# Kernel optimization log

Hardware: AMD Instinct MI355X
Metric: run time of the kernel (lower is better)

The kernel has to match this reference:

```python
import jax, jax.numpy as jnp
import numpy as np

M, K, N = 1024, 8192, 8192
PACK = 16  # 16 two-bit codes per int32 word


def _pack_ternary(codes):
    # codes: (N, K) int32 with values in {0,1,3} -> (N, K//16) int32
    c = codes.reshape(N, K // PACK, PACK).astype(jnp.uint32)
    shifts = (jnp.arange(PACK, dtype=jnp.uint32) * 2)
    packed = jnp.sum(c << shifts, axis=-1, dtype=jnp.uint32)
    return jax.lax.bitcast_convert_type(packed, jnp.int32)


def setup_inputs() -> dict:
    key = jax.random.key(0)
    kx, kw, kb = jax.random.split(key, 3)
    x = jax.random.normal(kx, (M, K), dtype=jnp.float16)
    # ternary codes drawn from {0,1,3} (code 2 is unused by the format)
    vals = jnp.array([0, 1, 3], dtype=jnp.int32)
    codes = vals[jax.random.randint(kw, (N, K), 0, 3)]
    packed_w = _pack_ternary(codes)
    bias = jax.random.normal(kb, (N,), dtype=jnp.float16)
    return {"x": x, "packed_w": packed_w, "bias": bias}


def _unpack(packed_w):
    # (N, K//16) int32 -> (N, K) fp16 weights with values in {0,1,3}
    shifts = jnp.arange(PACK, dtype=jnp.int32) * 2
    w = (packed_w[:, :, None] >> shifts) & 3  # mask keeps low 2 bits even with arithmetic shift
    return w.reshape(packed_w.shape[0], -1).astype(jnp.float16)


def reference(x, packed_w, bias):
    w = _unpack(packed_w)  # (N, K)
    # Y = X W^T + b, fp32 accumulation as in the CUDA/Triton GEMM, fp16 output
    y = jnp.einsum('mk,nk->mn', x, w, preferred_element_type=jnp.float32)
    y = y.astype(jnp.float16) + bias
    return y
```

## Files before the change

### kernel.cpp

```cpp
#include <hip/hip_runtime.h>
#include <hip/hip_fp16.h>
#include <stdint.h>

#define M_DIM 1024
#define N_DIM 8192
#define K_DIM 8192
#define KP    (K_DIM / 16)

#define BM 128
#define BN 128
#define BK 64
#define NTHREADS 256
#define B_STRIDE 144

#define MT_STRIDE 2097152
#define KT_STRIDE 16384

typedef _Float16 half8   __attribute__((ext_vector_type(8)));
typedef __fp16   fp16x2  __attribute__((ext_vector_type(2)));
typedef float    f32x4   __attribute__((ext_vector_type(4)));
typedef float    f32x16  __attribute__((ext_vector_type(16)));

__device__ __forceinline__ uint32_t cvt2(float a, float b) {
  fp16x2 p = __builtin_amdgcn_cvt_pkrtz(a, b);
  return __builtin_bit_cast(uint32_t, p);
}

__device__ __forceinline__ half8 dec_frag(uint32_t word, uint32_t sh) {
  const uint32_t T = 0x42063C00u;
  uint32_t h  = (word >> sh) & 0xFFFFu;
  uint32_t W  = (h & 0x3333u) | ((h << 14) & 0x33330000u);
  uint32_t c0 = __builtin_amdgcn_perm(0u, W, 0x04040200u);
  uint32_t c1 = __builtin_amdgcn_perm(0u, W, 0x04040301u);
  uint32_t s0 = (c0 * 0x1001u) & 0x03030303u;
  uint32_t s1 = (c1 * 0x1001u) & 0x03030303u;
  uint32_t P0 = __builtin_amdgcn_perm(0u, T, s0);
  uint32_t P1 = __builtin_amdgcn_perm(0u, T, s1);
  uint4 v;
  v.x = __builtin_amdgcn_perm(P0, 0u, 0x05000400u);
  v.y = __builtin_amdgcn_perm(P0, 0u, 0x07000600u);
  v.z = __builtin_amdgcn_perm(P1, 0u, 0x05000400u);
  v.w = __builtin_amdgcn_perm(P1, 0u, 0x07000600u);
  return __builtin_bit_cast(half8, v);
}

__global__ __launch_bounds__(256)
void cvt_x_t(const float* __restrict__ x, char* __restrict__ xhT) {
  __shared__ __align__(16) char st[16384];
  const int b  = blockIdx.x;
  const int mt = b >> 7, kt = b & 127;
  const int t  = threadIdx.x;
#pragma unroll
  for (int p = 0; p < 8; ++p) {
    int f   = t + 256 * p;
    int R   = f >> 4;
    int cc4 = f & 15;
    float4 v = *(const float4*)(x + (size_t)(mt * 128 + R) * K_DIM + kt * 64 + cc4 * 4);
    uint32_t w0 = cvt2(v.x, v.y), w1 = cvt2(v.z, v.w);
    int c8 = cc4 >> 1, hh = cc4 & 1;
    int i32 = R >> 5, r = R & 31, ks = c8 >> 1, q = c8 & 1;
    *(uint2*)(st + i32 * 4096 + ks * 1024 + q * 512 + r * 16 + hh * 8) = make_uint2(w0, w1);
  }
  __syncthreads();
  char* outb = xhT + (size_t)mt * MT_STRIDE + (size_t)kt * KT_STRIDE;
#pragma unroll
  for (int e = 0; e < 4; ++e) {
    int d = (e * 256 + t) * 16;
    *(uint4*)(outb + d) = *(const uint4*)(st + d);
  }
}

__global__ __launch_bounds__(NTHREADS, 2)
void ternary_gemm_dc(const char* __restrict__ xhT,
                     const int*  __restrict__ pw,
                     const float* __restrict__ bias,
                     float*       __restrict__ out) {
  __shared__ __align__(16) char stg[2 * 2048];

  const int tid  = threadIdx.x;
  const int lane = tid & 63;
  const int w    = tid >> 6;
  const int wm   = w >> 1, wn = w & 1;
  const int bid  = blockIdx.x;
  const int mt   = bid & 7;
  const int bm   = mt * BM;
  const int bn   = (bid >> 3) * BN;

  const char* pA[2];
#pragma unroll
  for (int i = 0; i < 2; ++i)
    pA[i] = xhT + (size_t)mt * MT_STRIDE + (wm * 2 + i) * 4096 + lane * 16;

  const int rT = tid >> 1, hT = tid & 1;
  const int2* gB = (const int2*)pw + (size_t)(bn + rT) * (KP / 2) + hT;
  const int stOff = rT * 16 + hT * 8;

  int rowOff[2];
#pragma unroll
  for (int j = 0; j < 2; ++j)
    rowOff[j] = (wn * 64 + j * 32 + (lane & 31)) * 16;
  const uint32_t sh = (lane >> 5) * 16;

  f32x16 acc[2][2];
#pragma unroll
  for (int i = 0; i < 2; ++i)
#pragma unroll
    for (int j = 0; j < 2; ++j) acc[i][j] = (f32x16)(0.f);

  const int NT = K_DIM / BK;

  *(int2*)(stg + stOff) = gB[0];
  half8 aA[2][4], aB[2][4];
#pragma unroll
  for (int i = 0; i < 2; ++i)
#pragma unroll
    for (int ks = 0; ks < 4; ++ks)
      aA[i][ks] = *(const half8*)(pA[i] + ks * 1024);
#pragma unroll
  for (int i = 0; i < 2; ++i) pA[i] += KT_STRIDE;
  int2 wcur = gB[2];
  __syncthreads();

  auto step = [&](half8 (&aC)[2][4], half8 (&aN)[2][4], int cur, int kt) {
#pragma unroll
    for (int i = 0; i < 2; ++i)
#pragma unroll
      for (int ks = 0; ks < 4; ++ks)
        aN[i][ks] = *(const half8*)(pA[i] + ks * 1024);
    if (kt < NT - 2) {
#pragma unroll
      for (int i = 0; i < 2; ++i) pA[i] += KT_STRIDE;
    }
    int kn2 = (kt + 2 < NT) ? (kt + 2) : (NT - 1);
    int2 wnxt = gB[kn2 * 2];

    uint32_t wr0[4], wr1[4];
    *(uint4*)wr0 = *(const uint4*)(stg + cur * 2048 + rowOff[0]);
    *(uint4*)wr1 = *(const uint4*)(stg + cur * 2048 + rowOff[1]);
    *(int2*)(stg + (cur ^ 1) * 2048 + stOff) = wcur;

#pragma unroll
    for (int ks = 0; ks < 4; ++ks) {
      half8 bf0 = dec_frag(wr0[ks], sh);
      half8 bf1 = dec_frag(wr1[ks], sh);
      acc[0][0] = __builtin_amdgcn_mfma_f32_32x32x16_f16(aC[0][ks], bf0, acc[0][0], 0, 0, 0);
      acc[0][1] = __builtin_amdgcn_mfma_f32_32x32x16_f16(aC[0][ks], bf1, acc[0][1], 0, 0, 0);
      acc[1][0] = __builtin_amdgcn_mfma_f32_32x32x16_f16(aC[1][ks], bf0, acc[1][0], 0, 0, 0);
      acc[1][1] = __builtin_amdgcn_mfma_f32_32x32x16_f16(aC[1][ks], bf1, acc[1][1], 0, 0, 0);
    }

    __syncthreads();
    wcur = wnxt;
  };

  for (int kt = 0; kt < NT; kt += 2) {
    step(aA, aB, 0, kt);
    step(aB, aA, 1, kt + 1);
  }

#pragma unroll
  for (int j = 0; j < 2; ++j) {
    int n = bn + wn * 64 + j * 32 + (lane & 31);
    __half hb = __float2half_rn(bias[n]);
#pragma unroll
    for (int i = 0; i < 2; ++i) {
      int mbase = bm + wm * 64 + i * 32 + 4 * (lane >> 5);
#pragma unroll
      for (int reg = 0; reg < 16; ++reg) {
        int m = mbase + (reg & 3) + 8 * (reg >> 2);
        __half hy = __float2half_rn(acc[i][j][reg]);
        out[(size_t)m * N_DIM + n] = __half2float(__hadd(hy, hb));
      }
    }
  }
}

__device__ __forceinline__ uint32_t unpack_pair16(uint32_t u, int p) {
  uint32_t c0 = (u >> (4 * p)) & 3u;
  uint32_t c1 = (u >> (4 * p + 2)) & 3u;
  uint32_t lo = (c0 & 1u) * 0x3C00u + (c0 >> 1) * 0x0600u;
  uint32_t hi = (c1 & 1u) * 0x3C00u + (c1 >> 1) * 0x0600u;
  return lo | (hi << 16);
}

__global__ __launch_bounds__(NTHREADS, 2)
void ternary_gemm(const float* __restrict__ x,
                  const int*   __restrict__ pw,
                  const float* __restrict__ bias,
                  float*       __restrict__ out) {
  __shared__ __align__(16) char AsB[128 * B_STRIDE];
  __shared__ __align__(16) char BsB[128 * B_STRIDE];

  const int tid  = threadIdx.x;
  const int lane = tid & 63;
  const int w    = tid >> 6;
  const int wm   = w >> 1, wn = w & 1;
  const int bid  = blockIdx.x;
  const int bm   = (bid & 7) * 128;
  const int bn   = (bid >> 3) * 128;

  const int rT = tid >> 1, hT = tid & 1;
  const float* gA = x + (size_t)(bm + rT) * K_DIM + hT * 32;
  char* const  lA = AsB + rT * B_STRIDE + hT * 64;
  const int2* gB = (const int2*)pw + (size_t)(bn + rT) * (KP / 2) + hT;
  char* dBp[4];
#pragma unroll
  for (int h = 0; h < 4; ++h)
    dBp[h] = BsB + rT * B_STRIDE + (hT * 4 + h) * 16;

  int offA[4][2], offB[4][2];
#pragma unroll
  for (int i = 0; i < 4; ++i)
#pragma unroll
    for (int ks = 0; ks < 2; ++ks) {
      int c = ks * 4 + (lane >> 4);
      offA[i][ks] = (wm * 64 + i * 16 + (lane & 15)) * B_STRIDE + c * 16;
      offB[i][ks] = (wn * 64 + i * 16 + (lane & 15)) * B_STRIDE + c * 16;
    }

  f32x4 acc[4][4];
#pragma unroll
  for (int i = 0; i < 4; ++i)
#pragma unroll
    for (int j = 0; j < 4; ++j)
      acc[i][j] = (f32x4){0.f, 0.f, 0.f, 0.f};

  const int NT = K_DIM / BK;
  for (int kt = 0; kt < NT; ++kt) {
    __syncthreads();
    int2 wcur = gB[kt * 2];
    float4 av[8];
#pragma unroll
    for (int v = 0; v < 8; ++v) av[v] = *(const float4*)(gA + kt * BK + v * 4);
    uint32_t d0[8], d1[8];
#pragma unroll
    for (int p = 0; p < 8; ++p) d0[p] = unpack_pair16((uint32_t)wcur.x, p);
#pragma unroll
    for (int p = 0; p < 8; ++p) d1[p] = unpack_pair16((uint32_t)wcur.y, p);
    *(uint4*)dBp[0] = make_uint4(d0[0], d0[1], d0[2], d0[3]);
    *(uint4*)dBp[1] = make_uint4(d0[4], d0[5], d0[6], d0[7]);
    *(uint4*)dBp[2] = make_uint4(d1[0], d1[1], d1[2], d1[3]);
    *(uint4*)dBp[3] = make_uint4(d1[4], d1[5], d1[6], d1[7]);
#pragma unroll
    for (int v = 0; v < 4; ++v) {
      uint4 aw;
      aw.x = cvt2(av[2 * v].x, av[2 * v].y);
      aw.y = cvt2(av[2 * v].z, av[2 * v].w);
      aw.z = cvt2(av[2 * v + 1].x, av[2 * v + 1].y);
      aw.w = cvt2(av[2 * v + 1].z, av[2 * v + 1].w);
      *(uint4*)(lA + v * 16) = aw;
    }
    __syncthreads();
#pragma unroll
    for (int ks = 0; ks < 2; ++ks) {
      half8 af[4], bf[4];
#pragma unroll
      for (int i = 0; i < 4; ++i) af[i] = *(const half8*)(AsB + offA[i][ks]);
#pragma unroll
      for (int j = 0; j < 4; ++j) bf[j] = *(const half8*)(BsB + offB[j][ks]);
#pragma unroll
      for (int i = 0; i < 4; ++i)
#pragma unroll
        for (int j = 0; j < 4; ++j)
          acc[i][j] = __builtin_amdgcn_mfma_f32_16x16x32_f16(af[i], bf[j], acc[i][j], 0, 0, 0);
    }
  }
#pragma unroll
  for (int j = 0; j < 4; ++j) {
    int n = bn + wn * 64 + j * 16 + (lane & 15);
    __half hb = __float2half_rn(bias[n]);
#pragma unroll
    for (int i = 0; i < 4; ++i) {
      int m0 = bm + wm * 64 + i * 16 + (lane >> 4) * 4;
#pragma unroll
      for (int r = 0; r < 4; ++r) {
        __half hy = __float2half_rn(acc[i][j][r]);
        out[(size_t)(m0 + r) * N_DIM + n] = __half2float(__hadd(hy, hb));
      }
    }
  }
}

extern "C" void kernel_launch(void* const* d_in, const int* in_sizes, int n_in,
                              void* d_out, int out_size, void* d_ws, size_t ws_size,
                              hipStream_t stream) {
  (void)in_sizes; (void)n_in; (void)out_size;
  const float* x    = (const float*)d_in[0];
  const int*   pwp  = (const int*)d_in[1];
  const float* bias = (const float*)d_in[2];
  float*       outp = (float*)d_out;

  const size_t need = (size_t)M_DIM * K_DIM * 2;
  if (ws_size >= need) {
    char* xhT = (char*)d_ws;
    cvt_x_t<<<8 * 128, 256, 0, stream>>>(x, xhT);
    dim3 grid((M_DIM / BM) * (N_DIM / BN));
    ternary_gemm_dc<<<grid, NTHREADS, 0, stream>>>(xhT, pwp, bias, outp);
  } else {
    dim3 grid((M_DIM / 128) * (N_DIM / 128));
    ternary_gemm<<<grid, NTHREADS, 0, stream>>>(x, pwp, bias, outp);
  }
}
```

Before: 237.0 us.

## Add weight repack pass and LDS-free single-wave 64x64 tile GEMM kernel

Adds a repack kernel that rearranges the packed ternary weights into a per-32-row-tile, per-k-step layout in workspace, so each lane can load its fragment directly. A new single-wavefront GEMM kernel with 64x64 tiles then streams both operands straight from global memory into registers with double buffering, removing shared memory staging and barriers. This adds an extra repack pass and workspace, and gives up the inter-wave data reuse of the 128x128 tile, so global and L2 traffic per output grows. The new path runs only when the workspace is large enough.

Measured after the change: 263.9 us. 1.11x slower.

```diff
diff --git a/kernel.cpp b/kernel.cpp
--- a/kernel.cpp
+++ b/kernel.cpp
@@ -7,14 +7,12 @@
 #define K_DIM 8192
 #define KP    (K_DIM / 16)
 
-#define BM 128
-#define BN 128
 #define BK 64
-#define NTHREADS 256
 #define B_STRIDE 144
 
 #define MT_STRIDE 2097152
 #define KT_STRIDE 16384
+#define BW_OFF    ((size_t)16 * 1024 * 1024)
 
 typedef _Float16 half8   __attribute__((ext_vector_type(8)));
 typedef __fp16   fp16x2  __attribute__((ext_vector_type(2)));
@@ -26,9 +24,8 @@
   return __builtin_bit_cast(uint32_t, p);
 }
 
-__device__ __forceinline__ half8 dec_frag(uint32_t word, uint32_t sh) {
+__device__ __forceinline__ half8 dec_h(uint32_t h) {
   const uint32_t T = 0x42063C00u;
-  uint32_t h  = (word >> sh) & 0xFFFFu;
   uint32_t W  = (h & 0x3333u) | ((h << 14) & 0x33330000u);
   uint32_t c0 = __builtin_amdgcn_perm(0u, W, 0x04040200u);
   uint32_t c1 = __builtin_amdgcn_perm(0u, W, 0x04040301u);
@@ -70,7 +67,124 @@
   }
 }
 
-__global__ __launch_bounds__(NTHREADS, 2)
+__global__ __launch_bounds__(256)
+void repack_w(const int* __restrict__ pw, char* __restrict__ bws) {
+  const int nt  = blockIdx.x & 255;
+  const int ktg = blockIdx.x >> 8;
+  const int r   = threadIdx.x & 31;
+  const int kto = threadIdx.x >> 5;
+  const int kt  = ktg * 8 + kto;
+  const int n   = nt * 32 + r;
+  int4 wv = *(const int4*)(pw + (size_t)n * KP + kt * 4);
+  uint32_t lo01 = __builtin_amdgcn_perm((uint32_t)wv.y, (uint32_t)wv.x, 0x05040100u);
+  uint32_t hi01 = __builtin_amdgcn_perm((uint32_t)wv.y, (uint32_t)wv.x, 0x07060302u);
+  uint32_t lo23 = __builtin_amdgcn_perm((uint32_t)wv.w, (uint32_t)wv.z, 0x05040100u);
+  uint32_t hi23 = __builtin_amdgcn_perm((uint32_t)wv.w, (uint32_t)wv.z, 0x07060302u);
+  char* base = bws + ((size_t)nt * 128 + kt) * 512;
+  *(uint2*)(base + r * 8)       = make_uint2(lo01, lo23);
+  *(uint2*)(base + 256 + r * 8) = make_uint2(hi01, hi23);
+}
+
+__global__ __launch_bounds__(64, 2)
+void ternary_gemm_nb(const char* __restrict__ xhT,
+                     const char* __restrict__ bws,
+                     const float* __restrict__ bias,
+                     float*       __restrict__ out) {
+  const int lane  = threadIdx.x;
+  const int bid   = blockIdx.x;
+  const int m_idx = ((bid & 7) << 1) | ((bid >> 3) & 1);
+  const int n_idx = bid >> 4;
+  const int m0 = m_idx * 64, n0 = n_idx * 64;
+
+  const char* pA[2];
+#pragma unroll
+  for (int i = 0; i < 2; ++i)
+    pA[i] = xhT + (size_t)(m_idx >> 1) * MT_STRIDE + ((m_idx & 1) * 2 + i) * 4096 + lane * 16;
+
+  const char* pB[2];
+#pragma unroll
+  for (int j = 0; j < 2; ++j)
+    pB[j] = bws + ((size_t)(n_idx * 2 + j) * 128) * 512 + lane * 8;
+
+  f32x16 acc[2][2];
+#pragma unroll
+  for (int i = 0; i < 2; ++i)
+#pragma unroll
+    for (int j = 0; j < 2; ++j) acc[i][j] = (f32x16)(0.f);
+
+  const int NT = K_DIM / BK;
+
+  half8 aA[2][4], aB[2][4];
+  uint2 bA[2], bB[2];
+#pragma unroll
+  for (int i = 0; i < 2; ++i)
+#pragma unroll
+    for (int ks = 0; ks < 4; ++ks)
+      aA[i][ks] = *(const half8*)(pA[i] + ks * 1024);
+#pragma unroll
+  for (int j = 0; j < 2; ++j) bA[j] = *(const uint2*)(pB[j]);
+#pragma unroll
+  for (int i = 0; i < 2; ++i) pA[i] += KT_STRIDE;
+#pragma unroll
+  for (int j = 0; j < 2; ++j) pB[j] += 512;
+
+  auto STEP = [&](half8 (&aC)[2][4], uint2 (&bC)[2],
+                  half8 (&aN)[2][4], uint2 (&bN)[2], int kt) {
+#pragma unroll
+    for (int i = 0; i < 2; ++i)
+#pragma unroll
+      for (int ks = 0; ks < 4; ++ks)
+        aN[i][ks] = *(const half8*)(pA[i] + ks * 1024);
+#pragma unroll
+    for (int j = 0; j < 2; ++j) bN[j] = *(const uint2*)(pB[j]);
+    if (kt < NT - 2) {
+#pragma unroll
+      for (int i = 0; i < 2; ++i) pA[i] += KT_STRIDE;
+#pragma unroll
+      for (int j = 0; j < 2; ++j) pB[j] += 512;
+    }
+#pragma unroll
+    for (int ks = 0; ks < 4; ++ks) {
+      uint32_t h0 = (ks & 2) ? (uint32_t)bC[0].y : (uint32_t)bC[0].x;
+      uint32_t h1 = (ks & 2) ? (uint32_t)bC[1].y : (uint32_t)bC[1].x;
+      h0 = (ks & 1) ? (h0 >> 16) : (h0 & 0xFFFFu);
+      h1 = (ks & 1) ? (h1 >> 16) : (h1 & 0xFFFFu);
+      half8 bf0 = dec_h(h0);
+      half8 bf1 = dec_h(h1);
+      acc[0][0] = __builtin_amdgcn_mfma_f32_32x32x16_f16(aC[0][ks], bf0, acc[0][0], 0, 0, 0);
+      acc[0][1] = __builtin_amdgcn_mfma_f32_32x32x16_f16(aC[0][ks], bf1, acc[0][1], 0, 0, 0);
+      acc[1][0] = __builtin_amdgcn_mfma_f32_32x32x16_f16(aC[1][ks], bf0, acc[1][0], 0, 0, 0);
+      acc[1][1] = __builtin_amdgcn_mfma_f32_32x32x16_f16(aC[1][ks], bf1, acc[1][1], 0, 0, 0);
+    }
+  };
+
+  for (int kt = 0; kt < NT; kt += 2) {
+    STEP(aA, bA, aB, bB, kt);
+    STEP(aB, bB, aA, bA, kt + 1);
+  }
+
+#pragma unroll
+  for (int j = 0; j < 2; ++j) {
+    int n = n0 + j * 32 + (lane & 31);
+    __half hb = __float2half_rn(bias[n]);
+#pragma unroll
+    for (int i = 0; i < 2; ++i) {
+      int mbase = m0 + i * 32 + 4 * (lane >> 5);
+#pragma unroll
+      for (int reg = 0; reg < 16; ++reg) {
+        int m = mbase + (reg & 3) + 8 * (reg >> 2);
+        __half hy = __float2half_rn(acc[i][j][reg]);
+        out[(size_t)m * N_DIM + n] = __half2float(__hadd(hy, hb));
+      }
+    }
+  }
+}
+
+__device__ __forceinline__ half8 dec_frag(uint32_t word, uint32_t sh) {
+  return dec_h((word >> sh) & 0xFFFFu);
+}
+
+__global__ __launch_bounds__(256, 2)
 void ternary_gemm_dc(const char* __restrict__ xhT,
                      const int*  __restrict__ pw,
                      const float* __restrict__ bias,
@@ -83,8 +197,8 @@
   const int wm   = w >> 1, wn = w & 1;
   const int bid  = blockIdx.x;
   const int mt   = bid & 7;
-  const int bm   = mt * BM;
-  const int bn   = (bid >> 3) * BN;
+  const int bm   = mt * 128;
+  const int bn   = (bid >> 3) * 128;
 
   const char* pA[2];
 #pragma unroll
@@ -148,7 +262,6 @@
       acc[1][0] = __builtin_amdgcn_mfma_f32_32x32x16_f16(aC[1][ks], bf0, acc[1][0], 0, 0, 0);
       acc[1][1] = __builtin_amdgcn_mfma_f32_32x32x16_f16(aC[1][ks], bf1, acc[1][1], 0, 0, 0);
     }
-
     __syncthreads();
     wcur = wnxt;
   };
@@ -183,7 +296,7 @@
   return lo | (hi << 16);
 }
 
-__global__ __launch_bounds__(NTHREADS, 2)
+__global__ __launch_bounds__(256, 2)
 void ternary_gemm(const float* __restrict__ x,
                   const int*   __restrict__ pw,
                   const float* __restrict__ bias,
@@ -290,14 +403,19 @@
   const float* bias = (const float*)d_in[2];
   float*       outp = (float*)d_out;
 
-  const size_t need = (size_t)M_DIM * K_DIM * 2;
-  if (ws_size >= need) {
+  const size_t need1 = (size_t)M_DIM * K_DIM * 2;
+  const size_t need2 = need1 + (size_t)16 * 1024 * 1024;
+  if (ws_size >= need2) {
+    char* xhT = (char*)d_ws;
+    char* bws = (char*)d_ws + BW_OFF;
+    cvt_x_t<<<8 * 128, 256, 0, stream>>>(x, xhT);
+    repack_w<<<256 * 16, 256, 0, stream>>>(pwp, bws);
+    ternary_gemm_nb<<<2048, 64, 0, stream>>>(xhT, bws, bias, outp);
+  } else if (ws_size >= need1) {
     char* xhT = (char*)d_ws;
     cvt_x_t<<<8 * 128, 256, 0, stream>>>(x, xhT);
-    dim3 grid((M_DIM / BM) * (N_DIM / BN));
-    ternary_gemm_dc<<<grid, NTHREADS, 0, stream>>>(xhT, pwp, bias, outp);
+    ternary_gemm_dc<<<512, 256, 0, stream>>>(xhT, pwp, bias, outp);
   } else {
-    dim3 grid((M_DIM / 128) * (N_DIM / 128));
-    ternary_gemm<<<grid, NTHREADS, 0, stream>>>(x, pwp, bias, outp);
-  }
-}
+    ternary_gemm<<<512, 256, 0, stream>>>(x, pwp, bias, outp);
+  }
+}
```
